# Kernel tuning notes

Measured on AMD Instinct MI355X. Metric: run time of the kernel, lower is better.

Reference implementation:

```python
import jax, jax.numpy as jnp
import numpy as np

N_FFT = 1024
HOP = 256


def _hann_periodic(n):
    # torch.hann_window default (periodic=True): 0.5*(1 - cos(2*pi*k/n))
    k = jnp.arange(n, dtype=jnp.float32)
    return 0.5 * (1.0 - jnp.cos(2.0 * jnp.pi * k / n))


def setup_inputs() -> dict:
    key = jax.random.key(0)
    x = jax.random.normal(key, (32, 2, 513, 1024, 2), dtype=jnp.float32)
    return {"x": x}


def reference(x):
    B, C, F, T, _ = x.shape
    n_fft = 2 * (F - 1)          # 1024
    hop = HOP
    # complex spectrum, frames along last-but-one axis -> (B*C, T, F)
    spec = jax.lax.complex(x[..., 0], x[..., 1])
    spec = spec.reshape(B * C, F, T).transpose(0, 2, 1)
    # torch.irfft(normalized=True) = true inverse * sqrt(n_fft)
    frames = jnp.fft.irfft(spec, n=n_fft, axis=-1) * np.float32(np.sqrt(n_fft))
    frames = frames * _hann_periodic(n_fft)[None, None, :]  # (BC, T, n_fft)
    # vectorized overlap-add (scatter-add)
    L = n_fft + hop * (T - 1)
    idx = jnp.arange(T)[:, None] * hop + jnp.arange(n_fft)[None, :]  # (T, n_fft)
    y = jnp.zeros((B * C, L), dtype=x.dtype).at[:, idx].add(frames)
    y = y[:, n_fft // 2:]
    coeff = n_fft / float(hop) / 2.0
    return (y / coeff).reshape(B, C, -1)
```

## Files before the change

### kernel.cpp

```cpp
#include <hip/hip_runtime.h>
#include <math.h>

#define NFFT 1024
#define HOP 256
#define NFREQ 513
#define TFRAMES 1024
#define NT_TILE 16
#define LOUT  262400
#define TILE_SAMPS 4864
#define NPAIR 2432

__device__ __forceinline__ float2 cadd(float2 a, float2 b){ return make_float2(a.x+b.x, a.y+b.y); }
__device__ __forceinline__ float2 csub(float2 a, float2 b){ return make_float2(a.x-b.x, a.y-b.y); }
__device__ __forceinline__ float2 muli(float2 a){ return make_float2(-a.y, a.x); }
__device__ __forceinline__ float2 cmul(float2 a, float2 b){
    return make_float2(a.x*b.x - a.y*b.y, a.x*b.y + a.y*b.x);
}

__device__ __forceinline__ void radix8_inv(float2& v0, float2& v1, float2& v2, float2& v3,
                                           float2& v4, float2& v5, float2& v6, float2& v7) {
    const float C = 0.70710678118654752f;
    float2 a0 = cadd(v0, v4), a1 = csub(v0, v4);
    float2 a2 = cadd(v2, v6), a3 = csub(v2, v6);
    float2 b0 = cadd(v1, v5), b1 = csub(v1, v5);
    float2 b2 = cadd(v3, v7), b3 = csub(v3, v7);
    float2 E0 = cadd(a0, a2), E2 = csub(a0, a2);
    float2 E1 = cadd(a1, muli(a3)), E3 = csub(a1, muli(a3));
    float2 O0 = cadd(b0, b2), O2 = csub(b0, b2);
    float2 O1 = cadd(b1, muli(b3)), O3 = csub(b1, muli(b3));
    float2 T1 = make_float2(C*(O1.x - O1.y),  C*(O1.x + O1.y));
    float2 T2 = muli(O2);
    float2 T3 = make_float2(-C*(O3.x + O3.y), C*(O3.x - O3.y));
    v0 = cadd(E0, O0); v4 = csub(E0, O0);
    v1 = cadd(E1, T1); v5 = csub(E1, T1);
    v2 = cadd(E2, T2); v6 = csub(E2, T2);
    v3 = cadd(E3, T3); v7 = csub(E3, T3);
}

__device__ __forceinline__ float2 twget(const float2* Tw, int m) {
    float2 t = Tw[m & 255];
    float s = (m & 256) ? -1.f : 1.f;
    return make_float2(s * t.x, s * t.y);
}

__device__ __forceinline__ int zpos(int n) {
    int blk = n >> 6;
    return blk * 64 + ((n & 63) ^ ((9 * blk) & 63));
}

__global__ __launch_bounds__(512, 4) void istft_kernel(const float2* __restrict__ x,
                                                       float* __restrict__ out) {
    __shared__ float2 Zc[8 * 512];
    __shared__ float2 OA[NPAIR];
    __shared__ float2 Tw[256];

    const int tid  = threadIdx.x;
    const int bc   = blockIdx.y;
    const int tile = blockIdx.x;
    const int t0   = tile * NT_TILE;
    const int S0   = t0 * HOP;

    if (tid < 256) {
        float s, c;
        __sincosf((float)tid * (6.283185307179586f / 512.f), &s, &c);
        Tw[tid] = make_float2(c, s);
    }
    #pragma unroll
    for (int r = 0; r < 5; ++r) { int p = tid + 512 * r; if (p < NPAIR) OA[p] = make_float2(0.f, 0.f); }
    __syncthreads();

    const int f     = tid >> 6;
    const int lane6 = tid & 63;
    const int fbase = f << 9;
    const int fx    = f << 1;

    const float HR = 0.99998117528260111f, HI = 0.00613588464915448f;

    for (int half = 0; half < 2; ++half) {
        {
            const int kg = tid >> 3, tt = tid & 7;
            const int tg = t0 + half * 8 + tt;
            const long baseIn = (long)bc * ((long)NFREQ * TFRAMES);
            const int wbase = tt << 9;
            const int fxw = tt << 1;
            #pragma unroll
            for (int i = 0; i < 5; ++i) {
                int kp = kg + 64 * i;
                if (kp <= 256) {
                    float2 A = x[baseIn + (long)kp * TFRAMES + tg];
                    float2 B = x[baseIn + (long)(512 - kp) * TFRAMES + tg];
                    if (kp == 0) { A.y = 0.f; B.y = 0.f; }
                    float2 tw = Tw[kp >> 1];
                    if (kp & 1) tw = make_float2(tw.x * HR - tw.y * HI, tw.x * HI + tw.y * HR);
                    float d2r = A.x - B.x, d2i = A.y + B.y;
                    float o2r = tw.x * d2r - tw.y * d2i, o2i = tw.x * d2i + tw.y * d2r;
                    float s2r = A.x + B.x, s2i = A.y - B.y;
                    Zc[wbase + (zpos(kp) ^ fxw)] = make_float2(0.5f * (s2r - o2i), 0.5f * (s2i + o2r));
                    if (kp >= 1 && kp <= 255)
                        Zc[wbase + (zpos(512 - kp) ^ fxw)] = make_float2(0.5f * (s2r + o2i), 0.5f * (o2r - s2i));
                }
            }
        }
        __syncthreads();

        {
            const int j = lane6, jx = lane6 ^ fx, zb = fbase;
            float2 v0 = Zc[zb +       (jx ^  0)];
            float2 v1 = Zc[zb +  64 + (jx ^  9)];
            float2 v2 = Zc[zb + 128 + (jx ^ 18)];
            float2 v3 = Zc[zb + 192 + (jx ^ 27)];
            float2 v4 = Zc[zb + 256 + (jx ^ 36)];
            float2 v5 = Zc[zb + 320 + (jx ^ 45)];
            float2 v6 = Zc[zb + 384 + (jx ^ 54)];
            float2 v7 = Zc[zb + 448 + (jx ^ 63)];
            radix8_inv(v0, v1, v2, v3, v4, v5, v6, v7);
            Zc[zb +       (jx ^  0)] = v0;
            Zc[zb +  64 + (jx ^  9)] = cmul(v1, twget(Tw, j));
            Zc[zb + 128 + (jx ^ 18)] = cmul(v2, twget(Tw, 2 * j));
            Zc[zb + 192 + (jx ^ 27)] = cmul(v3, twget(Tw, 3 * j));
            Zc[zb + 256 + (jx ^ 36)] = cmul(v4, twget(Tw, 4 * j));
            Zc[zb + 320 + (jx ^ 45)] = cmul(v5, twget(Tw, 5 * j));
            Zc[zb + 384 + (jx ^ 54)] = cmul(v6, twget(Tw, 6 * j));
            Zc[zb + 448 + (jx ^ 63)] = cmul(v7, twget(Tw, 7 * j));
        }
        {
            const int b = lane6 >> 3, jp = lane6 & 7;
            const int sw = ((9 * b) & 63) ^ fx, bb = fbase + 64 * b;
            float2 v0 = Zc[bb + ((jp     ) ^ sw)];
            float2 v1 = Zc[bb + ((jp +  8) ^ sw)];
            float2 v2 = Zc[bb + ((jp + 16) ^ sw)];
            float2 v3 = Zc[bb + ((jp + 24) ^ sw)];
            float2 v4 = Zc[bb + ((jp + 32) ^ sw)];
            float2 v5 = Zc[bb + ((jp + 40) ^ sw)];
            float2 v6 = Zc[bb + ((jp + 48) ^ sw)];
            float2 v7 = Zc[bb + ((jp + 56) ^ sw)];
            radix8_inv(v0, v1, v2, v3, v4, v5, v6, v7);
            const int m1 = 8 * jp;
            Zc[bb + ((jp     ) ^ sw)] = v0;
            Zc[bb + ((jp +  8) ^ sw)] = cmul(v1, twget(Tw, m1));
            Zc[bb + ((jp + 16) ^ sw)] = cmul(v2, twget(Tw, 2 * m1));
            Zc[bb + ((jp + 24) ^ sw)] = cmul(v3, twget(Tw, 3 * m1));
            Zc[bb + ((jp + 32) ^ sw)] = cmul(v4, twget(Tw, 4 * m1));
            Zc[bb + ((jp + 40) ^ sw)] = cmul(v5, twget(Tw, 5 * m1));
            Zc[bb + ((jp + 48) ^ sw)] = cmul(v6, twget(Tw, 6 * m1));
            Zc[bb + ((jp + 56) ^ sw)] = cmul(v7, twget(Tw, 7 * m1));
        }
        {
            const int b = lane6 >> 3, g = lane6 & 7;
            const int sw = ((9 * b) & 63) ^ fx, bb = fbase + 64 * b, g8 = 8 * g;
            float2 v0 = Zc[bb + ((g8    ) ^ sw)];
            float2 v1 = Zc[bb + ((g8 + 1) ^ sw)];
            float2 v2 = Zc[bb + ((g8 + 2) ^ sw)];
            float2 v3 = Zc[bb + ((g8 + 3) ^ sw)];
            float2 v4 = Zc[bb + ((g8 + 4) ^ sw)];
            float2 v5 = Zc[bb + ((g8 + 5) ^ sw)];
            float2 v6 = Zc[bb + ((g8 + 6) ^ sw)];
            float2 v7 = Zc[bb + ((g8 + 7) ^ sw)];
            radix8_inv(v0, v1, v2, v3, v4, v5, v6, v7);
            Zc[bb + ((g8    ) ^ sw)] = v0;
            Zc[bb + ((g8 + 1) ^ sw)] = v1;
            Zc[bb + ((g8 + 2) ^ sw)] = v2;
            Zc[bb + ((g8 + 3) ^ sw)] = v3;
            Zc[bb + ((g8 + 4) ^ sw)] = v4;
            Zc[bb + ((g8 + 5) ^ sw)] = v5;
            Zc[bb + ((g8 + 6) ^ sw)] = v6;
            Zc[bb + ((g8 + 7) ^ sw)] = v7;
        }
        __syncthreads();

        {
            const int h8 = half * 8;
            #pragma unroll
            for (int r = 0; r < 3; ++r) {
                int pi = (half ? 1024 : 0) + tid + 512 * r;
                if (pi < (half ? NPAIR : 1408)) {
                    int slh = pi >> 7;
                    int tlo = max(slh - 3, h8), thi = min(slh, h8 + 7);
                    int m0  = pi - (tlo << 7);
                    int k0  = m0 & 7;
                    int hi  = ((m0 >> 3) & 7) << 3;
                    int k2v = m0 >> 6;
                    int sw9 = (9 * k0) & 63;
                    float2 t0c = Tw[m0 & 255];
                    float sg = (m0 & 256) ? -1.f : 1.f;
                    float ce = sg * t0c.x, se = sg * t0c.y;
                    float ae = 0.f, ao = 0.f;
                    int cb = ((tlo - h8) << 9) + (k0 << 6);
                    for (int fr = tlo - h8; fr <= thi - h8; ++fr) {
                        int low = ((hi | k2v) ^ sw9) ^ (fr << 1);
                        float2 zz = Zc[cb + low];
                        float co = ce * HR - se * HI;
                        ae += zz.x * (1.f - ce);
                        ao += zz.y * (1.f - co);
                        float nc = se; se = -ce; ce = nc;
                        k2v -= 2; cb += 512;
                    }
                    float2 o = OA[pi];
                    o.x += ae * 0.015625f;
                    o.y += ao * 0.015625f;
                    OA[pi] = o;
                }
            }
        }
        __syncthreads();
    }

    #pragma unroll
    for (int r = 0; r < 5; ++r) {
        int pi = tid + 512 * r;
        if (pi < NPAIR) {
            int sl = pi << 1;
            int s  = S0 + sl;
            float2 v = OA[pi];
            if (pi >= 384 && pi < 2048) {
                reinterpret_cast<float2*>(out)[(bc * LOUT + (s - 512)) >> 1] = v;
            } else if (s >= 512) {
                atomicAdd(&out[bc * LOUT + (s - 512)], v.x);
                atomicAdd(&out[bc * LOUT + (s - 511)], v.y);
            }
        }
    }
}

extern "C" void kernel_launch(void* const* d_in, const int* in_sizes, int n_in,
                              void* d_out, int out_size, void* d_ws, size_t ws_size,
                              hipStream_t stream) {
    const float2* x = (const float2*)d_in[0];
    float* out = (float*)d_out;
    (void)in_sizes; (void)n_in; (void)d_ws; (void)ws_size;

    hipMemsetAsync(d_out, 0, (size_t)out_size * sizeof(float), stream);

    dim3 grid(TFRAMES / NT_TILE, 64);
    dim3 block(512);
    istft_kernel<<<grid, block, 0, stream>>>(x, out);
}
```

Baseline: 148.9 us.

## Halve frames per block and write overlap-add results directly to global

Cuts the frame tile from 16 to 8 per block, which removes the two-half loop and the shared-memory overlap-add accumulator. Each thread now writes its summed samples straight to the output, using plain stores for interior samples and atomics for the edges. The grid doubles and shared memory per block shrinks, which may allow more resident blocks. In exchange, a larger share of output samples sits in tile-overlap regions and needs global atomics (about 1.5 KB of each 2.75 KB tile instead of 1.5 KB of 4.75 KB).

```diff
diff --git a/kernel.cpp b/kernel.cpp
--- a/kernel.cpp
+++ b/kernel.cpp
@@ -5,10 +5,9 @@
 #define HOP 256
 #define NFREQ 513
 #define TFRAMES 1024
-#define NT_TILE 16
+#define NT_TILE 8
 #define LOUT  262400
-#define TILE_SAMPS 4864
-#define NPAIR 2432
+#define NPAIR 1408
 
 __device__ __forceinline__ float2 cadd(float2 a, float2 b){ return make_float2(a.x+b.x, a.y+b.y); }
 __device__ __forceinline__ float2 csub(float2 a, float2 b){ return make_float2(a.x-b.x, a.y-b.y); }
@@ -51,7 +50,6 @@
 __global__ __launch_bounds__(512, 4) void istft_kernel(const float2* __restrict__ x,
                                                        float* __restrict__ out) {
     __shared__ float2 Zc[8 * 512];
-    __shared__ float2 OA[NPAIR];
     __shared__ float2 Tw[256];
 
     const int tid  = threadIdx.x;
@@ -65,8 +63,6 @@
         __sincosf((float)tid * (6.283185307179586f / 512.f), &s, &c);
         Tw[tid] = make_float2(c, s);
     }
-    #pragma unroll
-    for (int r = 0; r < 5; ++r) { int p = tid + 512 * r; if (p < NPAIR) OA[p] = make_float2(0.f, 0.f); }
     __syncthreads();
 
     const int f     = tid >> 6;
@@ -76,147 +72,132 @@
 
     const float HR = 0.99998117528260111f, HI = 0.00613588464915448f;
 
-    for (int half = 0; half < 2; ++half) {
-        {
-            const int kg = tid >> 3, tt = tid & 7;
-            const int tg = t0 + half * 8 + tt;
-            const long baseIn = (long)bc * ((long)NFREQ * TFRAMES);
-            const int wbase = tt << 9;
-            const int fxw = tt << 1;
-            #pragma unroll
-            for (int i = 0; i < 5; ++i) {
-                int kp = kg + 64 * i;
-                if (kp <= 256) {
-                    float2 A = x[baseIn + (long)kp * TFRAMES + tg];
-                    float2 B = x[baseIn + (long)(512 - kp) * TFRAMES + tg];
-                    if (kp == 0) { A.y = 0.f; B.y = 0.f; }
-                    float2 tw = Tw[kp >> 1];
-                    if (kp & 1) tw = make_float2(tw.x * HR - tw.y * HI, tw.x * HI + tw.y * HR);
-                    float d2r = A.x - B.x, d2i = A.y + B.y;
-                    float o2r = tw.x * d2r - tw.y * d2i, o2i = tw.x * d2i + tw.y * d2r;
-                    float s2r = A.x + B.x, s2i = A.y - B.y;
-                    Zc[wbase + (zpos(kp) ^ fxw)] = make_float2(0.5f * (s2r - o2i), 0.5f * (s2i + o2r));
-                    if (kp >= 1 && kp <= 255)
-                        Zc[wbase + (zpos(512 - kp) ^ fxw)] = make_float2(0.5f * (s2r + o2i), 0.5f * (o2r - s2i));
-                }
+    {
+        const int kg = tid >> 3, tt = tid & 7;
+        const int tg = t0 + tt;
+        const long baseIn = (long)bc * ((long)NFREQ * TFRAMES);
+        const int wbase = tt << 9;
+        const int fxw = tt << 1;
+        #pragma unroll
+        for (int i = 0; i < 5; ++i) {
+            int kp = kg + 64 * i;
+            if (kp <= 256) {
+                float2 A = x[baseIn + (long)kp * TFRAMES + tg];
+                float2 B = x[baseIn + (long)(512 - kp) * TFRAMES + tg];
+                if (kp == 0) { A.y = 0.f; B.y = 0.f; }
+                float2 tw = Tw[kp >> 1];
+                if (kp & 1) tw = make_float2(tw.x * HR - tw.y * HI, tw.x * HI + tw.y * HR);
+                float d2r = A.x - B.x, d2i = A.y + B.y;
+                float o2r = tw.x * d2r - tw.y * d2i, o2i = tw.x * d2i + tw.y * d2r;
+                float s2r = A.x + B.x, s2i = A.y - B.y;
+                Zc[wbase + (zpos(kp) ^ fxw)] = make_float2(0.5f * (s2r - o2i), 0.5f * (s2i + o2r));
+                if (kp >= 1 && kp <= 255)
+                    Zc[wbase + (zpos(512 - kp) ^ fxw)] = make_float2(0.5f * (s2r + o2i), 0.5f * (o2r - s2i));
             }
         }
-        __syncthreads();
-
-        {
-            const int j = lane6, jx = lane6 ^ fx, zb = fbase;
-            float2 v0 = Zc[zb +       (jx ^  0)];
-            float2 v1 = Zc[zb +  64 + (jx ^  9)];
-            float2 v2 = Zc[zb + 128 + (jx ^ 18)];
-            float2 v3 = Zc[zb + 192 + (jx ^ 27)];
-            float2 v4 = Zc[zb + 256 + (jx ^ 36)];
-            float2 v5 = Zc[zb + 320 + (jx ^ 45)];
-            float2 v6 = Zc[zb + 384 + (jx ^ 54)];
-            float2 v7 = Zc[zb + 448 + (jx ^ 63)];
-            radix8_inv(v0, v1, v2, v3, v4, v5, v6, v7);
-            Zc[zb +       (jx ^  0)] = v0;
-            Zc[zb +  64 + (jx ^  9)] = cmul(v1, twget(Tw, j));
-            Zc[zb + 128 + (jx ^ 18)] = cmul(v2, twget(Tw, 2 * j));
-            Zc[zb + 192 + (jx ^ 27)] = cmul(v3, twget(Tw, 3 * j));
-            Zc[zb + 256 + (jx ^ 36)] = cmul(v4, twget(Tw, 4 * j));
-            Zc[zb + 320 + (jx ^ 45)] = cmul(v5, twget(Tw, 5 * j));
-            Zc[zb + 384 + (jx ^ 54)] = cmul(v6, twget(Tw, 6 * j));
-            Zc[zb + 448 + (jx ^ 63)] = cmul(v7, twget(Tw, 7 * j));
-        }
-        {
-            const int b = lane6 >> 3, jp = lane6 & 7;
-            const int sw = ((9 * b) & 63) ^ fx, bb = fbase + 64 * b;
-            float2 v0 = Zc[bb + ((jp     ) ^ sw)];
-            float2 v1 = Zc[bb + ((jp +  8) ^ sw)];
-            float2 v2 = Zc[bb + ((jp + 16) ^ sw)];
-            float2 v3 = Zc[bb + ((jp + 24) ^ sw)];
-            float2 v4 = Zc[bb + ((jp + 32) ^ sw)];
-            float2 v5 = Zc[bb + ((jp + 40) ^ sw)];
-            float2 v6 = Zc[bb + ((jp + 48) ^ sw)];
-            float2 v7 = Zc[bb + ((jp + 56) ^ sw)];
-            radix8_inv(v0, v1, v2, v3, v4, v5, v6, v7);
-            const int m1 = 8 * jp;
-            Zc[bb + ((jp     ) ^ sw)] = v0;
-            Zc[bb + ((jp +  8) ^ sw)] = cmul(v1, twget(Tw, m1));
-            Zc[bb + ((jp + 16) ^ sw)] = cmul(v2, twget(Tw, 2 * m1));
-            Zc[bb + ((jp + 24) ^ sw)] = cmul(v3, twget(Tw, 3 * m1));
-            Zc[bb + ((jp + 32) ^ sw)] = cmul(v4, twget(Tw, 4 * m1));
-            Zc[bb + ((jp + 40) ^ sw)] = cmul(v5, twget(Tw, 5 * m1));
-            Zc[bb + ((jp + 48) ^ sw)] = cmul(v6, twget(Tw, 6 * m1));
-            Zc[bb + ((jp + 56) ^ sw)] = cmul(v7, twget(Tw, 7 * m1));
-        }
-        {
-            const int b = lane6 >> 3, g = lane6 & 7;
-            const int sw = ((9 * b) & 63) ^ fx, bb = fbase + 64 * b, g8 = 8 * g;
-            float2 v0 = Zc[bb + ((g8    ) ^ sw)];
-            float2 v1 = Zc[bb + ((g8 + 1) ^ sw)];
-            float2 v2 = Zc[bb + ((g8 + 2) ^ sw)];
-            float2 v3 = Zc[bb + ((g8 + 3) ^ sw)];
-            float2 v4 = Zc[bb + ((g8 + 4) ^ sw)];
-            float2 v5 = Zc[bb + ((g8 + 5) ^ sw)];
-            float2 v6 = Zc[bb + ((g8 + 6) ^ sw)];
-            float2 v7 = Zc[bb + ((g8 + 7) ^ sw)];
-            radix8_inv(v0, v1, v2, v3, v4, v5, v6, v7);
-            Zc[bb + ((g8    ) ^ sw)] = v0;
-            Zc[bb + ((g8 + 1) ^ sw)] = v1;
-            Zc[bb + ((g8 + 2) ^ sw)] = v2;
-            Zc[bb + ((g8 + 3) ^ sw)] = v3;
-            Zc[bb + ((g8 + 4) ^ sw)] = v4;
-            Zc[bb + ((g8 + 5) ^ sw)] = v5;
-            Zc[bb + ((g8 + 6) ^ sw)] = v6;
-            Zc[bb + ((g8 + 7) ^ sw)] = v7;
-        }
-        __syncthreads();
-
-        {
-            const int h8 = half * 8;
-            #pragma unroll
-            for (int r = 0; r < 3; ++r) {
-                int pi = (half ? 1024 : 0) + tid + 512 * r;
-                if (pi < (half ? NPAIR : 1408)) {
-                    int slh = pi >> 7;
-                    int tlo = max(slh - 3, h8), thi = min(slh, h8 + 7);
-                    int m0  = pi - (tlo << 7);
-                    int k0  = m0 & 7;
-                    int hi  = ((m0 >> 3) & 7) << 3;
-                    int k2v = m0 >> 6;
-                    int sw9 = (9 * k0) & 63;
-                    float2 t0c = Tw[m0 & 255];
-                    float sg = (m0 & 256) ? -1.f : 1.f;
-                    float ce = sg * t0c.x, se = sg * t0c.y;
-                    float ae = 0.f, ao = 0.f;
-                    int cb = ((tlo - h8) << 9) + (k0 << 6);
-                    for (int fr = tlo - h8; fr <= thi - h8; ++fr) {
-                        int low = ((hi | k2v) ^ sw9) ^ (fr << 1);
-                        float2 zz = Zc[cb + low];
-                        float co = ce * HR - se * HI;
-                        ae += zz.x * (1.f - ce);
-                        ao += zz.y * (1.f - co);
-                        float nc = se; se = -ce; ce = nc;
-                        k2v -= 2; cb += 512;
-                    }
-                    float2 o = OA[pi];
-                    o.x += ae * 0.015625f;
-                    o.y += ao * 0.015625f;
-                    OA[pi] = o;
+    }
+    __syncthreads();
+
+    {
+        const int j = lane6, jx = lane6 ^ fx, zb = fbase;
+        float2 v0 = Zc[zb +       (jx ^  0)];
+        float2 v1 = Zc[zb +  64 + (jx ^  9)];
+        float2 v2 = Zc[zb + 128 + (jx ^ 18)];
+        float2 v3 = Zc[zb + 192 + (jx ^ 27)];
+        float2 v4 = Zc[zb + 256 + (jx ^ 36)];
+        float2 v5 = Zc[zb + 320 + (jx ^ 45)];
+        float2 v6 = Zc[zb + 384 + (jx ^ 54)];
+        float2 v7 = Zc[zb + 448 + (jx ^ 63)];
+        radix8_inv(v0, v1, v2, v3, v4, v5, v6, v7);
+        Zc[zb +       (jx ^  0)] = v0;
+        Zc[zb +  64 + (jx ^  9)] = cmul(v1, twget(Tw, j));
+        Zc[zb + 128 + (jx ^ 18)] = cmul(v2, twget(Tw, 2 * j));
+        Zc[zb + 192 + (jx ^ 27)] = cmul(v3, twget(Tw, 3 * j));
+        Zc[zb + 256 + (jx ^ 36)] = cmul(v4, twget(Tw, 4 * j));
+        Zc[zb + 320 + (jx ^ 45)] = cmul(v5, twget(Tw, 5 * j));
+        Zc[zb + 384 + (jx ^ 54)] = cmul(v6, twget(Tw, 6 * j));
+        Zc[zb + 448 + (jx ^ 63)] = cmul(v7, twget(Tw, 7 * j));
+    }
+    {
+        const int b = lane6 >> 3, jp = lane6 & 7;
+        const int sw = ((9 * b) & 63) ^ fx, bb = fbase + 64 * b;
+        float2 v0 = Zc[bb + ((jp     ) ^ sw)];
+        float2 v1 = Zc[bb + ((jp +  8) ^ sw)];
+        float2 v2 = Zc[bb + ((jp + 16) ^ sw)];
+        float2 v3 = Zc[bb + ((jp + 24) ^ sw)];
+        float2 v4 = Zc[bb + ((jp + 32) ^ sw)];
+        float2 v5 = Zc[bb + ((jp + 40) ^ sw)];
+        float2 v6 = Zc[bb + ((jp + 48) ^ sw)];
+        float2 v7 = Zc[bb + ((jp + 56) ^ sw)];
+        radix8_inv(v0, v1, v2, v3, v4, v5, v6, v7);
+        const int m1 = 8 * jp;
+        Zc[bb + ((jp     ) ^ sw)] = v0;
+        Zc[bb + ((jp +  8) ^ sw)] = cmul(v1, twget(Tw, m1));
+        Zc[bb + ((jp + 16) ^ sw)] = cmul(v2, twget(Tw, 2 * m1));
+        Zc[bb + ((jp + 24) ^ sw)] = cmul(v3, twget(Tw, 3 * m1));
+        Zc[bb + ((jp + 32) ^ sw)] = cmul(v4, twget(Tw, 4 * m1));
+        Zc[bb + ((jp + 40) ^ sw)] = cmul(v5, twget(Tw, 5 * m1));
+        Zc[bb + ((jp + 48) ^ sw)] = cmul(v6, twget(Tw, 6 * m1));
+        Zc[bb + ((jp + 56) ^ sw)] = cmul(v7, twget(Tw, 7 * m1));
+    }
+    {
+        const int b = lane6 >> 3, g = lane6 & 7;
+        const int sw = ((9 * b) & 63) ^ fx, bb = fbase + 64 * b, g8 = 8 * g;
+        float2 v0 = Zc[bb + ((g8    ) ^ sw)];
+        float2 v1 = Zc[bb + ((g8 + 1) ^ sw)];
+        float2 v2 = Zc[bb + ((g8 + 2) ^ sw)];
+        float2 v3 = Zc[bb + ((g8 + 3) ^ sw)];
+        float2 v4 = Zc[bb + ((g8 + 4) ^ sw)];
+        float2 v5 = Zc[bb + ((g8 + 5) ^ sw)];
+        float2 v6 = Zc[bb + ((g8 + 6) ^ sw)];
+        float2 v7 = Zc[bb + ((g8 + 7) ^ sw)];
+        radix8_inv(v0, v1, v2, v3, v4, v5, v6, v7);
+        Zc[bb + ((g8    ) ^ sw)] = v0;
+        Zc[bb + ((g8 + 1) ^ sw)] = v1;
+        Zc[bb + ((g8 + 2) ^ sw)] = v2;
+        Zc[bb + ((g8 + 3) ^ sw)] = v3;
+        Zc[bb + ((g8 + 4) ^ sw)] = v4;
+        Zc[bb + ((g8 + 5) ^ sw)] = v5;
+        Zc[bb + ((g8 + 6) ^ sw)] = v6;
+        Zc[bb + ((g8 + 7) ^ sw)] = v7;
+    }
+    __syncthreads();
+
+    {
+        #pragma unroll
+        for (int r = 0; r < 3; ++r) {
+            int pi = tid + 512 * r;
+            if (pi < NPAIR) {
+                int slh = pi >> 7;
+                int tlo = max(slh - 3, 0), thi = min(slh, 7);
+                int m0  = pi - (tlo << 7);
+                int k0  = m0 & 7;
+                int hi  = ((m0 >> 3) & 7) << 3;
+                int k2v = m0 >> 6;
+                int sw9 = (9 * k0) & 63;
+                float2 t0c = Tw[m0 & 255];
+                float sg = (m0 & 256) ? -1.f : 1.f;
+                float ce = sg * t0c.x, se = sg * t0c.y;
+                float ae = 0.f, ao = 0.f;
+                int cb = (tlo << 9) + (k0 << 6);
+                for (int fr = tlo; fr <= thi; ++fr) {
+                    int low = ((hi | k2v) ^ sw9) ^ (fr << 1);
+                    float2 zz = Zc[cb + low];
+                    float co = ce * HR - se * HI;
+                    ae += zz.x * (1.f - ce);
+                    ao += zz.y * (1.f - co);
+                    float nc = se; se = -ce; ce = nc;
+                    k2v -= 2; cb += 512;
                 }
-            }
-        }
-        __syncthreads();
-    }
-
-    #pragma unroll
-    for (int r = 0; r < 5; ++r) {
-        int pi = tid + 512 * r;
-        if (pi < NPAIR) {
-            int sl = pi << 1;
-            int s  = S0 + sl;
-            float2 v = OA[pi];
-            if (pi >= 384 && pi < 2048) {
-                reinterpret_cast<float2*>(out)[(bc * LOUT + (s - 512)) >> 1] = v;
-            } else if (s >= 512) {
-                atomicAdd(&out[bc * LOUT + (s - 512)], v.x);
-                atomicAdd(&out[bc * LOUT + (s - 511)], v.y);
+                ae *= 0.015625f; ao *= 0.015625f;
+                int s = S0 + (pi << 1);
+                if (pi >= 384 && pi < 1024) {
+                    reinterpret_cast<float2*>(out)[(bc * LOUT + (s - 512)) >> 1] =
+                        make_float2(ae, ao);
+                } else if (s >= 512) {
+                    atomicAdd(&out[bc * LOUT + (s - 512)], ae);
+                    atomicAdd(&out[bc * LOUT + (s - 511)], ao);
+                }
             }
         }
     }
```

Result: faster. 129.5 us (-13.0%).
